# Performance work log

Hardware: AMD Instinct MI355X
Metric: run time of the kernel (lower is better)

## Reference

```python
import jax, jax.numpy as jnp
import numpy as np
from jax.scipy.special import logsumexp

B, L, M, D = 8192, 1024, 128, 2  # batch, hilbert.size, bond dim, local_size
MACHINE_POW = 2


def setup_inputs() -> dict:
    key = jax.random.key(0)
    k1, k2 = jax.random.split(key)
    # configurations in the zero-magnetization sector: each row is a permutation
    # of L//2 zeros and L//2 ones (constrained HomogeneousHilbert)
    base = jnp.tile(jnp.arange(D, dtype=jnp.int32), L // D)  # (L,)
    inputs = jax.vmap(lambda k: jax.random.permutation(k, base))(jax.random.split(k1, B))
    # variational parameters epsilon: (local_size, M, size); centered at 1 so the
    # length-L multiplicative cache chain stays in fp32 range
    epsilon = 1.0 + 0.02 * jax.random.normal(k2, (D, M, L), dtype=jnp.float32)
    return {"inputs": inputs, "epsilon": epsilon}


def _conditionals(inputs, epsilon):
    # inputs: (B, L) int in [0, D); epsilon: (D, M, L)
    Bn, Ln = inputs.shape
    Dn, Mn, _ = epsilon.shape
    half = Ln // 2

    def scan_fun(carry, index):
        cache, n_spins = carry                       # (B, D, M), (B, D)
        prev = inputs[:, (index - 1) % Ln]           # (B,) previous-site state
        params_i = epsilon[:, :, index]              # (D, M)
        # irregular gather: cache[b, prev[b], :]
        gathered = jnp.take_along_axis(cache, prev[:, None, None], axis=1)[:, 0, :]  # (B, M)
        prods = params_i[None, :, :] * gathered[:, None, :]  # (B, D, M)
        log_psi = jnp.sum(prods, axis=-1)            # (B, D) sum over bond dim
        n_spins = jnp.where(index > 0,
                            n_spins + jax.nn.one_hot(prev, Dn, dtype=jnp.int32),
                            n_spins)
        # zero-magnetization renormalization: -inf once a local state is exhausted
        renorm = jnp.log(jnp.heaviside((half - n_spins).astype(log_psi.dtype), 0.0))
        return (prods, n_spins), log_psi + renorm

    cache0 = jnp.ones((Bn, Dn, Mn), epsilon.dtype)
    n0 = jnp.zeros((Bn, Dn), jnp.int32)
    _, log_psi = jax.lax.scan(scan_fun, (cache0, n0), jnp.arange(Ln))
    return jnp.transpose(log_psi, (1, 0, 2))  # (B, L, D)


def reference(inputs, epsilon):
    lp = _conditionals(inputs, epsilon)  # (B, L, D)
    # normalize conditionals over local states (machine_pow = 2)
    lp = lp - (1.0 / MACHINE_POW) * logsumexp(MACHINE_POW * lp, axis=-1, keepdims=True)
    # pick the log-conditional of the actual configuration at each site
    sel = jnp.take_along_axis(lp, inputs[:, :, None], axis=2)[:, :, 0]  # (B, L)
    # n_symm = 1 (default apply_symmetries): symmetrized logsumexp is identity
    return jnp.sum(sel, axis=1)  # (B,) log_psi
```

## Files before the change

kernel.cpp:

```cpp
#include <hip/hip_runtime.h>
#include <hip/hip_fp16.h>

typedef unsigned long long u64;
typedef unsigned int uint32;
typedef short short8 __attribute__((ext_vector_type(8)));
typedef float f32x4 __attribute__((ext_vector_type(4)));
typedef _Float16 h2 __attribute__((ext_vector_type(2)));

#define B_N 8192
#define L_N 1024
#define M_N 128
#define HALF_N 512

#define OFF_W16  0
#define OFF_R16  0x40000
#define OFF_BITS 0x80000
#define OFF_LR   0x180000
#define OFF_T    0x1C0000
#define OFF_RQ   0x200000

#define PACK_BLK 2048
#define PACK_IT  16
#define EPS_BLK  32
#define ZERO_BLK 32

__device__ __forceinline__ unsigned short f32_bf16(float f) {
    union { float f; unsigned u; } x; x.f = f;
    unsigned u = x.u + 0x7FFFu + ((x.u >> 16) & 1u);
    return (unsigned short)(u >> 16);
}

__device__ __forceinline__ float fdot2(h2 a, h2 b, float c) {
#if __has_builtin(__builtin_amdgcn_fdot2)
    return __builtin_amdgcn_fdot2(a, b, c, false);
#else
    return (float)a[0] * (float)b[0] + (float)a[1] * (float)b[1] + c;
#endif
}

__device__ __forceinline__ uint32 fas_u(float f) { union { float f; uint32 u; } x; x.f = f; return x.u; }
__device__ __forceinline__ float uas_f(uint32 u) { union { uint32 u; float f; } x; x.u = u; return x.f; }

__device__ __forceinline__ float exp2_n(float x) {
#if __has_builtin(__builtin_amdgcn_exp2f)
    return __builtin_amdgcn_exp2f(x);
#else
    return exp2f(x);
#endif
}
__device__ __forceinline__ float log2_n(float x) {
#if __has_builtin(__builtin_amdgcn_logf)
    return __builtin_amdgcn_logf(x);
#else
    return __log2f(x);
#endif
}
__device__ __forceinline__ uint32 bfe1(uint32 v, int off) {
#if __has_builtin(__builtin_amdgcn_sbfe)
    return (uint32)__builtin_amdgcn_sbfe((int)v, off, 1);
#else
    return (uint32)((int)(v << (31 - off)) >> 31);
#endif
}

template<int CTRL>
__device__ __forceinline__ float dpp_add(float x, float y) {
    union { float f; int i; } a, r;
    a.f = y;
    r.i = __builtin_amdgcn_update_dpp(0, a.i, CTRL, 0xF, 0xF, true);
    return x + r.f;
}

union HU { uint32 u; __half2 hh; h2 v2; };

__global__ __launch_bounds__(256) void k_prep(const int* __restrict__ inp,
        const float* __restrict__ eps, u64* __restrict__ bits,
        _Float16* __restrict__ w16, _Float16* __restrict__ r16,
        unsigned short* __restrict__ lrT, float* __restrict__ out) {
    int bid = blockIdx.x;
    if (bid < PACK_BLK) {
        int g = bid * 256 + threadIdx.x;
        const int stride = PACK_BLK * 256;
        #pragma unroll 4
        for (int it = 0; it < PACK_IT; ++it) {
            int v = inp[g];
            u64 m = __ballot(v != 0);
            if ((threadIdx.x & 63) == 0) bits[g >> 6] = m;
            g += stride;
        }
        return;
    }
    bid -= PACK_BLK;
    if (bid < EPS_BLK) {
        int wid = threadIdx.x >> 6, lane = threadIdx.x & 63;
        int m = bid * 4 + wid;
        const float* e0 = eps + (size_t)m * L_N + lane * 16;
        const float* e1 = eps + (size_t)(M_N + m) * L_N + lane * 16;
        float a[16], b[16];
        #pragma unroll
        for (int j = 0; j < 16; j += 4) {
            *(float4*)&a[j] = *(const float4*)&e0[j];
            *(float4*)&b[j] = *(const float4*)&e1[j];
        }
        float local = 1.f;
        #pragma unroll
        for (int j = 0; j < 16; ++j) local *= a[j];
        float sc = local;
        #pragma unroll
        for (int d = 1; d < 64; d <<= 1) {
            float up = __shfl_up(sc, d);
            if (lane >= d) sc *= up;
        }
        float prev = __shfl_up(sc, 1);
        float E = (lane == 0) ? 1.f : prev;
        int i0 = lane * 16;
        #pragma unroll
        for (int j = 0; j < 16; ++j) {
            float rat = b[j] / a[j];
            w16[(size_t)(i0 + j) * M_N + m] = (_Float16)(E * (a[j] - b[j]));
            r16[(size_t)(i0 + j) * M_N + m] = (_Float16)(rat - 1.f);
            lrT[(size_t)m * L_N + i0 + j] = f32_bf16(__log2f(rat));
            E *= a[j];
        }
        return;
    }
    bid -= EPS_BLK;
    if (bid < ZERO_BLK) {
        out[bid * 256 + threadIdx.x] = 0.f;
    }
}

template<int CN>
__global__ __launch_bounds__(256) void k_slog2(const u64* __restrict__ bits,
        const unsigned short* __restrict__ lrT, _Float16* __restrict__ Rq,
        int* __restrict__ T) {
    if (blockIdx.x >= 1024) {
        int b = (blockIdx.x - 1024) * 256 + threadIdx.x;
        const u64* brow = bits + (size_t)b * 16;
        int n1 = 0, n0 = 0, Tv = 1024;
        for (int wd = 0; wd < 16; ++wd) {
            u64 x = brow[wd];
            int pc = __popcll(x);
            if (n1 + pc < HALF_N && n0 + (64 - pc) < HALF_N) {
                n1 += pc; n0 += 64 - pc;
                continue;
            }
            int found = 0;
            for (int k = 0; k < 64; ++k) {
                if (n1 >= HALF_N || n0 >= HALF_N) { Tv = wd * 64 + k; found = 1; break; }
                int sb = (int)((x >> k) & 1);
                n1 += sb; n0 += 1 - sb;
            }
            if (!found) Tv = (wd + 1) * 64;
            break;
        }
        T[b] = Tv;
        return;
    }
    int btile = blockIdx.x >> 1;
    int half = blockIdx.x & 1;
    int wid = threadIdx.x >> 6, lane = threadIdx.x & 63;
    int col = lane & 15, quad = lane >> 4;
    int m = (half * 4 + wid) * 16 + col;
    int b_row = btile * 16 + col;
    const u64* brow = bits + (size_t)b_row * 16;
    const unsigned short* lrow = lrT + (size_t)m * L_N;

    f32x4 cum = (f32x4){0.f, 0.f, 0.f, 0.f};

    for (int w = 0; w < 16; ++w) {
        u64 wv = brow[w];
        #pragma unroll
        for (int hf = 0; hf < 2; ++hf) {
            if (CN == 32 || hf == 0) {
                int cc = (CN == 32) ? (w * 2 + hf) : w;
                #pragma unroll
                for (int reg = 0; reg < 4; ++reg) {
                    int b = btile * 16 + quad * 4 + reg;
                    Rq[((size_t)cc * B_N + b) * M_N + m] = (_Float16)exp2_n(cum[reg]);
                }
            }
            short8 a;
            #pragma unroll
            for (int j = 0; j < 8; ++j)
                a[j] = (short)((((wv >> (hf * 32 + quad * 8 + j)) & 1) != 0) ? 0x3F80 : 0);
            union { uint4 u; short8 s; } bf;
            bf.u = *(const uint4*)(lrow + w * 64 + hf * 32 + quad * 8);
            cum = __builtin_amdgcn_mfma_f32_16x16x32_bf16(a, bf.s, cum, 0, 0, 0);
        }
    }
}

template<int CN>
__global__ __launch_bounds__(256) __attribute__((amdgpu_waves_per_eu(1, 4)))
void k_main(const u64* __restrict__ bits,
        const _Float16* __restrict__ w16, const _Float16* __restrict__ r16,
        const _Float16* __restrict__ Rq, const int* __restrict__ T,
        float* __restrict__ out) {
    constexpr int CHN = L_N / CN;
    constexpr int CSH = (CN == 16) ? 4 : 5;
    constexpr int NV  = (CHN * M_N) / (8 * 256);
    __shared__ _Float16 wbuf[CHN * M_N];
    __shared__ _Float16 rbuf[CHN * M_N];
    int c = blockIdx.x & (CN - 1);
    int bblk = blockIdx.x >> CSH;
    int lane = threadIdx.x & 63, wid = threadIdx.x >> 6;
    int s = lane & 7, grp = lane >> 3;
    int q = s & 3;
    int b0 = bblk * 128 + wid * 32 + grp * 4;

    {
        const uint4* sw = (const uint4*)(w16 + (size_t)c * CHN * M_N);
        const uint4* sr = (const uint4*)(r16 + (size_t)c * CHN * M_N);
        uint4* dw = (uint4*)wbuf; uint4* dr = (uint4*)rbuf;
        #pragma unroll
        for (int t = 0; t < NV; ++t) {
            dw[threadIdx.x + t * 256] = sw[threadIdx.x + t * 256];
            dr[threadIdx.x + t * 256] = sr[threadIdx.x + t * 256];
        }
    }

    HU R2[4][8];
    u64 wb[4];
    const int word0 = (c * CHN) >> 6;
    const int hs0 = (c * CHN >> 5) & 1;
    #pragma unroll
    for (int k = 0; k < 4; ++k) {
        int b = b0 + (q ^ k);
        union { uint4 v[2]; uint32 w[8]; } P;
        const uint4* src = (const uint4*)(Rq + ((size_t)c * B_N + b) * M_N + s * 16);
        P.v[0] = src[0]; P.v[1] = src[1];
        #pragma unroll
        for (int j = 0; j < 8; ++j) R2[k][j].u = P.w[j];
        wb[k] = bits[(size_t)b * 16 + word0];
    }
    int Tb = T[b0 + q];

    __syncthreads();

    const float LOG2E2 = 2.885390082f;
    const float NHL2 = -0.3465735903f;
    float sum = 0.f;
    #pragma unroll
    for (int h = 0; h < CHN / 32; ++h) {
        int sh = ((hs0 + h) & 1) * 32;
        uint32 wh[4];
        #pragma unroll
        for (int k = 0; k < 4; ++k) wh[k] = (uint32)(wb[k] >> sh);
        uint32 ows = ~wh[0];
        int rel = Tb - (c * CHN + h * 32);
        uint32 vmask = (rel <= 0) ? 0u : ((rel >= 32) ? 0xFFFFFFFFu : ((1u << rel) - 1u));

        for (int tt = 0; tt < 32; ++tt) {
            int base = (h * 32 + tt) * M_N + s * 16;
            union { uint4 q4[2]; uint32 w[8]; h2 v2[8]; } W, Rm;
            W.q4[0] = *(const uint4*)&wbuf[base];
            W.q4[1] = *((const uint4*)&wbuf[base] + 1);
            Rm.q4[0] = *(const uint4*)&rbuf[base];
            Rm.q4[1] = *((const uint4*)&rbuf[base] + 1);

            float d[4];
            #pragma unroll
            for (int k = 0; k < 4; ++k) {
                float acc = 0.f;
                #pragma unroll
                for (int j = 0; j < 8; ++j) acc = fdot2(R2[k][j].v2, W.v2[j], acc);
                d[k] = acc;
            }
            float xa = dpp_add<0xB1>(d[0], d[1]);
            float xb = dpp_add<0xB1>(d[2], d[3]);
            float uD = dpp_add<0x4E>(xa, xb);
            uD = dpp_add<0x104>(uD, uD);

            uint32 sgn = bfe1(ows, tt) & 0x80000000u;
            float y = uas_f(fas_u(uD) ^ sgn);
            float contr = NHL2 * log2_n(1.f + exp2_n(LOG2E2 * y));
            sum += uas_f(fas_u(contr) & bfe1(vmask, tt));

            #pragma unroll
            for (int k = 0; k < 4; ++k) {
                uint32 msk = bfe1(wh[k], tt);
                #pragma unroll
                for (int j = 0; j < 8; ++j) {
                    HU sel; sel.u = Rm.w[j] & msk;
                    R2[k][j].v2 += sel.v2 * R2[k][j].v2;
                }
            }
        }
    }
    if (s < 4) atomicAdd(&out[b0 + s], sum);
}

extern "C" void kernel_launch(void* const* d_in, const int* in_sizes, int n_in,
                              void* d_out, int out_size, void* d_ws, size_t ws_size,
                              hipStream_t stream) {
    const int*   inputs  = (const int*)d_in[0];
    const float* epsilon = (const float*)d_in[1];
    float* out = (float*)d_out;

    char* ws = (char*)d_ws;
    _Float16* w16 = (_Float16*)(ws + OFF_W16);
    _Float16* r16 = (_Float16*)(ws + OFF_R16);
    u64*   bits   = (u64*)  (ws + OFF_BITS);
    unsigned short* lrT = (unsigned short*)(ws + OFF_LR);
    int*   T      = (int*)  (ws + OFF_T);
    _Float16* Rq  = (_Float16*)(ws + OFF_RQ);

    k_prep<<<PACK_BLK + EPS_BLK + ZERO_BLK, 256, 0, stream>>>(
        inputs, epsilon, bits, w16, r16, lrT, out);

    const size_t need32 = (size_t)OFF_RQ + (size_t)32 * B_N * M_N * 2;
    if (ws_size >= need32) {
        k_slog2<32><<<1024 + 32, 256, 0, stream>>>(bits, lrT, Rq, T);
        k_main<32><<<(B_N / 128) * 32, 256, 0, stream>>>(bits, w16, r16, Rq, T, out);
    } else {
        k_slog2<16><<<1024 + 32, 256, 0, stream>>>(bits, lrT, Rq, T);
        k_main<16><<<(B_N / 128) * 16, 256, 0, stream>>>(bits, w16, r16, Rq, T, out);
    }
}
```

Baseline: 171.8 us.

## Process sites in pairs with precombined odd-site weights and pair update factors

The main loop now handles two sites per iteration. The odd site's weight vector is pre-multiplied by the even site's ratio when the even bit is set, so both dot products use the same R state. The running R vector is then updated once per pair with a precomputed combined factor chosen by the two-bit configuration. This halves the per-site multiplicative state updates and the dependency chain through R. In exchange it uses more shared memory, needs per-lane indexed LDS loads of 2-way and 4-way tables, and adds fp16 rounding from the product of ratios.

```diff
diff --git a/kernel.cpp b/kernel.cpp
--- a/kernel.cpp
+++ b/kernel.cpp
@@ -12,12 +12,13 @@
 #define M_N 128
 #define HALF_N 512
 
-#define OFF_W16  0
-#define OFF_R16  0x40000
-#define OFF_BITS 0x80000
-#define OFF_LR   0x180000
-#define OFF_T    0x1C0000
-#define OFF_RQ   0x200000
+#define OFF_WE   0x0
+#define OFF_WO   0x20000
+#define OFF_CMB  0x60000
+#define OFF_LR   0xE0000
+#define OFF_BITS 0x120000
+#define OFF_T    0x220000
+#define OFF_RQ   0x240000
 
 #define PACK_BLK 2048
 #define PACK_IT  16
@@ -60,6 +61,13 @@
     return (uint32)__builtin_amdgcn_sbfe((int)v, off, 1);
 #else
     return (uint32)((int)(v << (31 - off)) >> 31);
+#endif
+}
+__device__ __forceinline__ uint32 ubfe2(uint32 v, int off) {
+#if __has_builtin(__builtin_amdgcn_ubfe)
+    return (uint32)__builtin_amdgcn_ubfe((int)v, off, 2);
+#else
+    return (v >> off) & 3u;
 #endif
 }
 
@@ -75,7 +83,8 @@
 
 __global__ __launch_bounds__(256) void k_prep(const int* __restrict__ inp,
         const float* __restrict__ eps, u64* __restrict__ bits,
-        _Float16* __restrict__ w16, _Float16* __restrict__ r16,
+        _Float16* __restrict__ wE, _Float16* __restrict__ wO,
+        _Float16* __restrict__ cmb,
         unsigned short* __restrict__ lrT, float* __restrict__ out) {
     int bid = blockIdx.x;
     if (bid < PACK_BLK) {
@@ -114,12 +123,26 @@
         float prev = __shfl_up(sc, 1);
         float E = (lane == 0) ? 1.f : prev;
         int i0 = lane * 16;
+        float rat_e = 1.f;
         #pragma unroll
         for (int j = 0; j < 16; ++j) {
             float rat = b[j] / a[j];
-            w16[(size_t)(i0 + j) * M_N + m] = (_Float16)(E * (a[j] - b[j]));
-            r16[(size_t)(i0 + j) * M_N + m] = (_Float16)(rat - 1.f);
+            float w = E * (a[j] - b[j]);
             lrT[(size_t)m * L_N + i0 + j] = f32_bf16(__log2f(rat));
+            int u = (i0 + j) >> 1;
+            if ((j & 1) == 0) {
+                wE[(size_t)u * M_N + m] = (_Float16)w;
+                rat_e = rat;
+            } else {
+                _Float16* wo = wO + (size_t)u * 2 * M_N;
+                wo[m]       = (_Float16)w;
+                wo[M_N + m] = (_Float16)(w * rat_e);
+                _Float16* cr = cmb + (size_t)u * 4 * M_N;
+                cr[m]           = (_Float16)0.f;
+                cr[M_N + m]     = (_Float16)(rat_e - 1.f);
+                cr[2*M_N + m]   = (_Float16)(rat - 1.f);
+                cr[3*M_N + m]   = (_Float16)(rat_e * rat - 1.f);
+            }
             E *= a[j];
         }
         return;
@@ -193,15 +216,17 @@
 
 template<int CN>
 __global__ __launch_bounds__(256) __attribute__((amdgpu_waves_per_eu(1, 4)))
-void k_main(const u64* __restrict__ bits,
-        const _Float16* __restrict__ w16, const _Float16* __restrict__ r16,
+void k_main(const u64* __restrict__ bits, const _Float16* __restrict__ wE,
+        const _Float16* __restrict__ wO, const _Float16* __restrict__ cmb,
         const _Float16* __restrict__ Rq, const int* __restrict__ T,
         float* __restrict__ out) {
     constexpr int CHN = L_N / CN;
+    constexpr int PRS = CHN / 2;
     constexpr int CSH = (CN == 16) ? 4 : 5;
-    constexpr int NV  = (CHN * M_N) / (8 * 256);
-    __shared__ _Float16 wbuf[CHN * M_N];
-    __shared__ _Float16 rbuf[CHN * M_N];
+    constexpr int NE  = PRS * M_N / (8 * 256);
+    __shared__ _Float16 webuf[PRS * M_N];
+    __shared__ _Float16 wobuf[PRS * 2 * M_N];
+    __shared__ _Float16 cbuf [PRS * 4 * M_N];
     int c = blockIdx.x & (CN - 1);
     int bblk = blockIdx.x >> CSH;
     int lane = threadIdx.x & 63, wid = threadIdx.x >> 6;
@@ -210,14 +235,16 @@
     int b0 = bblk * 128 + wid * 32 + grp * 4;
 
     {
-        const uint4* sw = (const uint4*)(w16 + (size_t)c * CHN * M_N);
-        const uint4* sr = (const uint4*)(r16 + (size_t)c * CHN * M_N);
-        uint4* dw = (uint4*)wbuf; uint4* dr = (uint4*)rbuf;
-        #pragma unroll
-        for (int t = 0; t < NV; ++t) {
-            dw[threadIdx.x + t * 256] = sw[threadIdx.x + t * 256];
-            dr[threadIdx.x + t * 256] = sr[threadIdx.x + t * 256];
-        }
+        const uint4* se = (const uint4*)(wE  + (size_t)c * PRS * M_N);
+        const uint4* so = (const uint4*)(wO  + (size_t)c * PRS * 2 * M_N);
+        const uint4* sc = (const uint4*)(cmb + (size_t)c * PRS * 4 * M_N);
+        uint4* de = (uint4*)webuf; uint4* dd = (uint4*)wobuf; uint4* dc = (uint4*)cbuf;
+        #pragma unroll
+        for (int t = 0; t < NE; ++t)     de[threadIdx.x + t * 256] = se[threadIdx.x + t * 256];
+        #pragma unroll
+        for (int t = 0; t < 2 * NE; ++t) dd[threadIdx.x + t * 256] = so[threadIdx.x + t * 256];
+        #pragma unroll
+        for (int t = 0; t < 4 * NE; ++t) dc[threadIdx.x + t * 256] = sc[threadIdx.x + t * 256];
     }
 
     HU R2[4][8];
@@ -251,40 +278,66 @@
         int rel = Tb - (c * CHN + h * 32);
         uint32 vmask = (rel <= 0) ? 0u : ((rel >= 32) ? 0xFFFFFFFFu : ((1u << rel) - 1u));
 
-        for (int tt = 0; tt < 32; ++tt) {
-            int base = (h * 32 + tt) * M_N + s * 16;
-            union { uint4 q4[2]; uint32 w[8]; h2 v2[8]; } W, Rm;
-            W.q4[0] = *(const uint4*)&wbuf[base];
-            W.q4[1] = *((const uint4*)&wbuf[base] + 1);
-            Rm.q4[0] = *(const uint4*)&rbuf[base];
-            Rm.q4[1] = *((const uint4*)&rbuf[base] + 1);
-
-            float d[4];
+        #pragma unroll 2
+        for (int tt = 0; tt < 16; ++tt) {
+            int p = h * 16 + tt;
+            union U8 { uint4 q4[2]; uint32 w[8]; h2 v2[8]; __half2 hh[8]; };
+            U8 WEu;
+            const _Float16* web = &webuf[p * M_N + s * 16];
+            WEu.q4[0] = *(const uint4*)web;
+            WEu.q4[1] = *((const uint4*)web + 1);
+
+            uint32 cbo[4];
+            #pragma unroll
+            for (int k = 0; k < 4; ++k) cbo[k] = ubfe2(wh[k], 2 * tt);
+
+            float de[4];
             #pragma unroll
             for (int k = 0; k < 4; ++k) {
                 float acc = 0.f;
                 #pragma unroll
-                for (int j = 0; j < 8; ++j) acc = fdot2(R2[k][j].v2, W.v2[j], acc);
-                d[k] = acc;
-            }
-            float xa = dpp_add<0xB1>(d[0], d[1]);
-            float xb = dpp_add<0xB1>(d[2], d[3]);
-            float uD = dpp_add<0x4E>(xa, xb);
-            uD = dpp_add<0x104>(uD, uD);
-
-            uint32 sgn = bfe1(ows, tt) & 0x80000000u;
-            float y = uas_f(fas_u(uD) ^ sgn);
-            float contr = NHL2 * log2_n(1.f + exp2_n(LOG2E2 * y));
-            sum += uas_f(fas_u(contr) & bfe1(vmask, tt));
-
+                for (int j = 0; j < 8; ++j) acc = fdot2(R2[k][j].v2, WEu.v2[j], acc);
+                de[k] = acc;
+            }
+            float dd[4];
             #pragma unroll
             for (int k = 0; k < 4; ++k) {
-                uint32 msk = bfe1(wh[k], tt);
+                U8 WOu;
+                int ob = p * 2 * M_N + (int)((cbo[k] & 1u) << 7) + s * 16;
+                WOu.q4[0] = *(const uint4*)&wobuf[ob];
+                WOu.q4[1] = *((const uint4*)&wobuf[ob] + 1);
+                float acc = 0.f;
                 #pragma unroll
-                for (int j = 0; j < 8; ++j) {
-                    HU sel; sel.u = Rm.w[j] & msk;
-                    R2[k][j].v2 += sel.v2 * R2[k][j].v2;
-                }
+                for (int j = 0; j < 8; ++j) acc = fdot2(R2[k][j].v2, WOu.v2[j], acc);
+                dd[k] = acc;
+            }
+            float xe = dpp_add<0xB1>(de[0], de[1]);
+            float ye = dpp_add<0xB1>(de[2], de[3]);
+            float De = dpp_add<0x4E>(xe, ye);
+            De = dpp_add<0x104>(De, De);
+            float xo = dpp_add<0xB1>(dd[0], dd[1]);
+            float yo = dpp_add<0xB1>(dd[2], dd[3]);
+            float Do = dpp_add<0x4E>(xo, yo);
+            Do = dpp_add<0x104>(Do, Do);
+
+            uint32 sg0 = bfe1(ows, 2 * tt) & 0x80000000u;
+            float y0 = uas_f(fas_u(De) ^ sg0);
+            float c0 = NHL2 * log2_n(1.f + exp2_n(LOG2E2 * y0));
+            sum += uas_f(fas_u(c0) & bfe1(vmask, 2 * tt));
+            uint32 sg1 = bfe1(ows, 2 * tt + 1) & 0x80000000u;
+            float y1 = uas_f(fas_u(Do) ^ sg1);
+            float c1 = NHL2 * log2_n(1.f + exp2_n(LOG2E2 * y1));
+            sum += uas_f(fas_u(c1) & bfe1(vmask, 2 * tt + 1));
+
+            #pragma unroll
+            for (int k = 0; k < 4; ++k) {
+                U8 CMu;
+                int cb = p * 4 * M_N + (int)(cbo[k] << 7) + s * 16;
+                CMu.q4[0] = *(const uint4*)&cbuf[cb];
+                CMu.q4[1] = *((const uint4*)&cbuf[cb] + 1);
+                #pragma unroll
+                for (int j = 0; j < 8; ++j)
+                    R2[k][j].hh = __hfma2(CMu.hh[j], R2[k][j].hh, R2[k][j].hh);
             }
         }
     }
@@ -299,22 +352,23 @@
     float* out = (float*)d_out;
 
     char* ws = (char*)d_ws;
-    _Float16* w16 = (_Float16*)(ws + OFF_W16);
-    _Float16* r16 = (_Float16*)(ws + OFF_R16);
+    _Float16* wE  = (_Float16*)(ws + OFF_WE);
+    _Float16* wO  = (_Float16*)(ws + OFF_WO);
+    _Float16* cmb = (_Float16*)(ws + OFF_CMB);
+    unsigned short* lrT = (unsigned short*)(ws + OFF_LR);
     u64*   bits   = (u64*)  (ws + OFF_BITS);
-    unsigned short* lrT = (unsigned short*)(ws + OFF_LR);
     int*   T      = (int*)  (ws + OFF_T);
     _Float16* Rq  = (_Float16*)(ws + OFF_RQ);
 
     k_prep<<<PACK_BLK + EPS_BLK + ZERO_BLK, 256, 0, stream>>>(
-        inputs, epsilon, bits, w16, r16, lrT, out);
+        inputs, epsilon, bits, wE, wO, cmb, lrT, out);
 
     const size_t need32 = (size_t)OFF_RQ + (size_t)32 * B_N * M_N * 2;
     if (ws_size >= need32) {
         k_slog2<32><<<1024 + 32, 256, 0, stream>>>(bits, lrT, Rq, T);
-        k_main<32><<<(B_N / 128) * 32, 256, 0, stream>>>(bits, w16, r16, Rq, T, out);
+        k_main<32><<<(B_N / 128) * 32, 256, 0, stream>>>(bits, wE, wO, cmb, Rq, T, out);
     } else {
         k_slog2<16><<<1024 + 32, 256, 0, stream>>>(bits, lrT, Rq, T);
-        k_main<16><<<(B_N / 128) * 16, 256, 0, stream>>>(bits, w16, r16, Rq, T, out);
-    }
-}
+        k_main<16><<<(B_N / 128) * 16, 256, 0, stream>>>(bits, wE, wO, cmb, Rq, T, out);
+    }
+}
```

New measurement: 163.4 us. 4.9% less time.
